# Optimization experiments

Hardware: AMD Instinct MI355X
Metric: run time of the kernel (lower is better)

Reference implementation:

```python
import jax, jax.numpy as jnp
import numpy as np

B, F, E, V = 8192, 16, 32, 100000
D, H1, H2 = 8, 1024, 512
IN = F * E  # 512
EPS = 1e-5


def _bn(x, gamma, beta):
    # x: [D, B, H]; training-mode BatchNorm1d per domain over batch axis (biased var)
    mean = jnp.mean(x, axis=1, keepdims=True)
    var = jnp.mean((x - mean) ** 2, axis=1, keepdims=True)
    return (x - mean) * jax.lax.rsqrt(var + EPS) * gamma[:, None, :] + beta[:, None, :]


def setup_inputs() -> dict:
    key = jax.random.key(0)
    ks = jax.random.split(key, 12)
    feat_ids = jax.random.randint(ks[0], (B, F), 0, V)
    domain_id = jax.random.randint(ks[1], (B,), 0, D)
    emb_tables = jax.random.normal(ks[2], (F, V, E), jnp.float32) * 0.02
    s1 = 1.0 / np.sqrt(IN)
    s2 = 1.0 / np.sqrt(H1)
    s3 = 1.0 / np.sqrt(H2)
    return {
        "feat_ids": feat_ids,
        "domain_id": domain_id,
        "emb_tables": emb_tables,
        "W1": jax.random.uniform(ks[3], (D, H1, IN), jnp.float32, -s1, s1),
        "b1": jax.random.uniform(ks[4], (D, H1), jnp.float32, -s1, s1),
        "g1": jnp.ones((D, H1), jnp.float32),
        "be1": jnp.zeros((D, H1), jnp.float32),
        "W2": jax.random.uniform(ks[5], (D, H2, H1), jnp.float32, -s2, s2),
        "b2": jax.random.uniform(ks[6], (D, H2), jnp.float32, -s2, s2),
        "g2": jnp.ones((D, H2), jnp.float32),
        "be2": jnp.zeros((D, H2), jnp.float32),
        "W3": jax.random.uniform(ks[7], (D, H2), jnp.float32, -s3, s3),
        "b3": jax.random.uniform(ks[8], (D,), jnp.float32, -s3, s3),
    }


def reference(feat_ids, domain_id, emb_tables, W1, b1, g1, be1, W2, b2, g2, be2, W3, b3):
    # embedding lookup per feature then concat -> [B, F*E]
    emb = jax.vmap(lambda tab, ids: tab[ids], in_axes=(0, 1), out_axes=1)(emb_tables, feat_ids)
    emb = emb.reshape(B, IN)
    # all-domain redundant MLP (as in original torch code)
    h = jnp.einsum('bf,dhf->dbh', emb, W1) + b1[:, None, :]          # [D,B,H1]
    h = jax.nn.relu(_bn(h, g1, be1))
    h = jnp.einsum('dbh,dkh->dbk', h, W2) + b2[:, None, :]           # [D,B,H2]
    h = jax.nn.relu(_bn(h, g2, be2))
    out = jax.nn.sigmoid(jnp.einsum('dbk,dk->db', h, W3) + b3[:, None])  # [D,B]
    # mask-select the row matching each sample's domain
    final = jnp.take_along_axis(out.T, domain_id[:, None], axis=1)[:, 0]  # [B]
    return final
```

## Files before the change

kernel.cpp:

```cpp
#include <hip/hip_runtime.h>
#include <hip/hip_bf16.h>

#define B_SZ   8192
#define F_CNT  16
#define E_DIM  32
#define V_CNT  100000
#define D_CNT  8
#define H1     1024
#define H2     512
#define IN_DIM 512
#define EPS_BN 1e-5f
#define SNIFF_THRESH 32

typedef __attribute__((ext_vector_type(8))) unsigned short ushort8;
typedef __attribute__((ext_vector_type(8))) short          frag_ab;
typedef __attribute__((ext_vector_type(4))) float          frag_cd;
typedef __attribute__((ext_vector_type(4))) float          float4v;

__device__ inline unsigned short f2b(float f) {
    unsigned int u = __builtin_bit_cast(unsigned int, f);
    unsigned int r = u + 0x7FFFu + ((u >> 16) & 1u);
    return (unsigned short)(r >> 16);
}
__device__ inline float b2f(unsigned short b) {
    return __builtin_bit_cast(float, (unsigned int)b << 16);
}

__global__ void k_sniff(const unsigned short* __restrict__ w, int nwords,
                        int* __restrict__ cnt) {
    int t = threadIdx.x;
    int c = 0;
    for (int i = t; i < nwords; i += 256) {
        unsigned int e = (w[i] >> 7) & 0xFFu;
        if (e >= 0x88u) c++;
    }
    __shared__ int red[256];
    red[t] = c; __syncthreads();
    for (int s = 128; s > 0; s >>= 1) { if (t < s) red[t] += red[t + s]; __syncthreads(); }
    if (t == 0) atomicAdd(cnt, red[0]);
}

__global__ void k_convert(const void* __restrict__ src, unsigned short* __restrict__ dst,
                          long n, const int* __restrict__ cnt) {
    long i = (long)blockIdx.x * 256 + threadIdx.x;
    if (i >= n) return;
    if (*cnt > SNIFF_THRESH) dst[i] = f2b(((const float*)src)[i]);
    else                     dst[i] = ((const unsigned short*)src)[i];
}

__global__ void k_gather(const int* __restrict__ feat_ids,
                         const void* __restrict__ tables,
                         unsigned short* __restrict__ emb,
                         const int* __restrict__ cnt) {
    int tid = blockIdx.x * 256 + threadIdx.x;
    int b = tid >> 6;
    int c = tid & 63;
    int f = c >> 2;
    int id = feat_ids[b * F_CNT + f];
    long base = ((long)f * V_CNT + id) * E_DIM + (c & 3) * 8;
    ushort8 o;
    if (*cnt > SNIFF_THRESH) {
        const float* s = (const float*)tables + base;
        float4v v0 = *(const float4v*)s;
        float4v v1 = *(const float4v*)(s + 4);
#pragma unroll
        for (int i = 0; i < 4; i++) { o[i] = f2b(v0[i]); o[i + 4] = f2b(v1[i]); }
    } else {
        o = *(const ushort8*)((const unsigned short*)tables + base);
    }
    *(ushort8*)(emb + (long)b * IN_DIM + c * 8) = o;
}

__global__ __launch_bounds__(256, 2)
void k_gemm(const unsigned short* __restrict__ A,
            const unsigned short* __restrict__ W,
            unsigned short* __restrict__ C,
            int M, int N, int K, long aBatchStride, int d0) {
    const int z  = blockIdx.z;
    const int m0 = blockIdx.x * 128;
    const int n0 = blockIdx.y * 128;
    const unsigned short* Ad = A + (long)z * aBatchStride;
    const unsigned short* Wd = W + (long)(d0 + z) * N * K;

    __shared__ unsigned short As[128][40];
    __shared__ unsigned short Bs[128][40];

    const int t    = threadIdx.x;
    const int wave = t >> 6;
    const int lane = t & 63;
    const int wm   = (wave & 1) << 6;
    const int wn   = (wave >> 1) << 6;
    const int q    = lane >> 4;
    const int lr   = lane & 15;

    const int r0   = t >> 2;
    const int koff = (t & 3) * 8;

    const unsigned short* aP0 = Ad + (long)(m0 + r0)      * K + koff;
    const unsigned short* aP1 = Ad + (long)(m0 + r0 + 64) * K + koff;
    const unsigned short* wP0 = Wd + (long)(n0 + r0)      * K + koff;
    const unsigned short* wP1 = Wd + (long)(n0 + r0 + 64) * K + koff;

    frag_cd acc[4][4];
#pragma unroll
    for (int i = 0; i < 4; i++)
#pragma unroll
        for (int j = 0; j < 4; j++)
            acc[i][j] = (frag_cd){0.f, 0.f, 0.f, 0.f};

    for (int k0 = 0; k0 < K; k0 += 32) {
        ushort8 a0 = *(const ushort8*)aP0;
        ushort8 a1 = *(const ushort8*)aP1;
        ushort8 b0 = *(const ushort8*)wP0;
        ushort8 b1 = *(const ushort8*)wP1;
        aP0 += 32; aP1 += 32; wP0 += 32; wP1 += 32;
        *(ushort8*)&As[r0][koff]      = a0;
        *(ushort8*)&As[r0 + 64][koff] = a1;
        *(ushort8*)&Bs[r0][koff]      = b0;
        *(ushort8*)&Bs[r0 + 64][koff] = b1;
        __syncthreads();

        frag_ab af[4], bf[4];
#pragma unroll
        for (int i = 0; i < 4; i++) {
            af[i] = *(const frag_ab*)&As[wm + i * 16 + lr][q * 8];
            bf[i] = *(const frag_ab*)&Bs[wn + i * 16 + lr][q * 8];
        }
#pragma unroll
        for (int i = 0; i < 4; i++)
#pragma unroll
            for (int j = 0; j < 4; j++)
                acc[i][j] = __builtin_amdgcn_mfma_f32_16x16x32_bf16(af[i], bf[j], acc[i][j], 0, 0, 0);
        __syncthreads();
    }

    unsigned short* Cd = C + (long)z * M * N;
#pragma unroll
    for (int i = 0; i < 4; i++) {
        int row = m0 + wm + i * 16 + q * 4;
#pragma unroll
        for (int j = 0; j < 4; j++) {
            int col = n0 + wn + j * 16 + lr;
#pragma unroll
            for (int r = 0; r < 4; r++)
                Cd[(long)(row + r) * N + col] = f2b(acc[i][j][r]);
        }
    }
}

__global__ void k_stats(const unsigned short* __restrict__ P, int H,
                        float* __restrict__ gsum, float* __restrict__ gsq, int d0) {
    const int z   = blockIdx.z;
    const int j0  = blockIdx.x * 128;
    const int seg = blockIdx.y;
    const int t = threadIdx.x;
    const int c = t & 15, r = t >> 4;
    const unsigned short* base = P + ((long)z * B_SZ + seg * 1024) * H + j0 + c * 8;
    float s[8], q[8];
#pragma unroll
    for (int i = 0; i < 8; i++) { s[i] = 0.f; q[i] = 0.f; }
    for (int b = r; b < 1024; b += 16) {
        ushort8 v = *(const ushort8*)(base + (long)b * H);
#pragma unroll
        for (int i = 0; i < 8; i++) { float x = b2f(v[i]); s[i] += x; q[i] += x * x; }
    }
    __shared__ float red[16][128];
#pragma unroll
    for (int i = 0; i < 8; i++) red[r][c * 8 + i] = s[i];
    __syncthreads();
    if (t < 128) {
        float a = 0.f;
#pragma unroll
        for (int rr = 0; rr < 16; rr++) a += red[rr][t];
        atomicAdd(&gsum[(d0 + z) * H + j0 + t], a);
    }
    __syncthreads();
#pragma unroll
    for (int i = 0; i < 8; i++) red[r][c * 8 + i] = q[i];
    __syncthreads();
    if (t < 128) {
        float a = 0.f;
#pragma unroll
        for (int rr = 0; rr < 16; rr++) a += red[rr][t];
        atomicAdd(&gsq[(d0 + z) * H + j0 + t], a);
    }
}

__global__ void k_finalize(const float* __restrict__ gsum, const float* __restrict__ gsq,
                           const void* __restrict__ g, const void* __restrict__ be,
                           float* __restrict__ scale, float* __restrict__ shift, int n,
                           int gOff, const int* __restrict__ cnt) {
    int i = blockIdx.x * 256 + threadIdx.x;
    if (i >= n) return;
    float gv, bv;
    if (*cnt > SNIFF_THRESH) {
        gv = ((const float*)g)[gOff + i];
        bv = ((const float*)be)[gOff + i];
    } else {
        gv = b2f(((const unsigned short*)g)[gOff + i]);
        bv = b2f(((const unsigned short*)be)[gOff + i]);
    }
    float mean = gsum[i] * (1.0f / B_SZ);
    float var  = gsq[i] * (1.0f / B_SZ) - mean * mean;
    float sc   = gv * rsqrtf(var + EPS_BN);
    scale[i] = sc;
    shift[i] = bv - mean * sc;
}

__global__ void k_bn_apply(const unsigned short* __restrict__ P,
                           const float* __restrict__ scale, const float* __restrict__ shift,
                           unsigned short* __restrict__ Out, int H, int d0) {
    long tid = (long)blockIdx.x * 256 + threadIdx.x;
    long off = tid * 8;
    int j  = (int)(off % H);
    int dj = ((int)(off / ((long)B_SZ * H)) + d0) * H + j;
    ushort8 v = *(const ushort8*)(P + off);
    float4v sc0 = *(const float4v*)(scale + dj);
    float4v sc1 = *(const float4v*)(scale + dj + 4);
    float4v sh0 = *(const float4v*)(shift + dj);
    float4v sh1 = *(const float4v*)(shift + dj + 4);
    ushort8 o;
#pragma unroll
    for (int i = 0; i < 8; i++) {
        float scv = (i < 4) ? sc0[i] : sc1[i - 4];
        float shv = (i < 4) ? sh0[i] : sh1[i - 4];
        float x = b2f(v[i]) * scv + shv;
        o[i] = f2b(fmaxf(x, 0.f));
    }
    *(ushort8*)(Out + off) = o;
}

__global__ void k_final(const unsigned short* __restrict__ h2c,
                        const int* __restrict__ domain_id,
                        const float* __restrict__ scale2, const float* __restrict__ shift2,
                        const unsigned short* __restrict__ W3, const unsigned short* __restrict__ b3,
                        void* __restrict__ out, int d0, int nc,
                        const int* __restrict__ cnt) {
    int wave = threadIdx.x >> 6, lane = threadIdx.x & 63;
    int b = blockIdx.x * 4 + wave;
    int d = domain_id[b];
    if (d < d0 || d >= d0 + nc) return;
    int o = d * H2 + lane * 8;
    ushort8 v = *(const ushort8*)(h2c + ((long)(d - d0) * B_SZ + b) * H2 + lane * 8);
    ushort8 w = *(const ushort8*)(W3 + o);
    float sum = 0.f;
#pragma unroll
    for (int i = 0; i < 8; i++) {
        float x = b2f(v[i]) * scale2[o + i] + shift2[o + i];
        sum += fmaxf(x, 0.f) * b2f(w[i]);
    }
#pragma unroll
    for (int off = 32; off > 0; off >>= 1) sum += __shfl_xor(sum, off, 64);
    if (lane == 0) {
        float res = 1.f / (1.f + expf(-(sum + b2f(b3[d]))));
        if (*cnt > SNIFF_THRESH) ((float*)out)[b] = res;
        else                     ((unsigned short*)out)[b] = f2b(res);
    }
}

__global__ void k_zero(float* __restrict__ p, int n) {
    int i = blockIdx.x * 256 + threadIdx.x;
    if (i < n) p[i] = 0.f;
}

__global__ void k_sentinel(float* __restrict__ out, int n) {
    int i = blockIdx.x * 256 + threadIdx.x;
    if (i < n) out[i] = 0.25f;
}

extern "C" void kernel_launch(void* const* d_in, const int* in_sizes, int n_in,
                              void* d_out, int out_size, void* d_ws, size_t ws_size,
                              hipStream_t stream) {
    const int* feat_ids  = (const int*)d_in[0];
    const int* domain_id = (const int*)d_in[1];
    const void* tables = d_in[2];
    const void* W1  = d_in[3];
    const void* g1  = d_in[5];
    const void* be1 = d_in[6];
    const void* W2  = d_in[7];
    const void* g2  = d_in[9];
    const void* be2 = d_in[10];
    const void* W3  = d_in[11];
    const void* b3  = d_in[12];

    char* ws = (char*)d_ws;
    float* gsum1  = (float*)ws;
    float* gsq1   = gsum1 + 8192;
    float* gsum2  = gsq1 + 8192;
    float* gsq2   = gsum2 + 4096;
    float* scale1 = gsq2 + 4096;
    float* shift1 = scale1 + 8192;
    float* scale2 = shift1 + 8192;
    float* shift2 = scale2 + 4096;
    int*   cntF   = (int*)(shift2 + 4096);
    unsigned short* W1c = (unsigned short*)(ws + (1L  << 20));
    unsigned short* W2c = (unsigned short*)(ws + (9L  << 20));
    unsigned short* W3c = (unsigned short*)(ws + (17L << 20));
    unsigned short* b3c = W3c + D_CNT * H2;
    unsigned short* emb = (unsigned short*)(ws + (18L << 20));

    const long h1Elems = (long)B_SZ * H1;
    const long h2Elems = (long)B_SZ * H2;
    const long perDom  = (h1Elems + h2Elems) * 2;
    const long baseOff = 26L << 20;
    int NC = 0;
    for (int cand = 8; cand >= 1; cand >>= 1)
        if (baseOff + (long)cand * perDom <= (long)ws_size) { NC = cand; break; }
    if (NC == 0) {
        k_sentinel<<<dim3((out_size + 255) / 256), dim3(256), 0, stream>>>(
            (float*)d_out, out_size);
        return;
    }
    unsigned short* h1c = (unsigned short*)(ws + baseOff);
    unsigned short* h2c = h1c + (long)NC * h1Elems;

    k_zero<<<dim3(193), dim3(256), 0, stream>>>(gsum1, 49184);
    k_sniff<<<dim3(1), dim3(256), 0, stream>>>((const unsigned short*)W1, 4096, cntF);
    k_convert<<<dim3(16384), dim3(256), 0, stream>>>(W1, W1c, (long)D_CNT * H1 * IN_DIM, cntF);
    k_convert<<<dim3(16384), dim3(256), 0, stream>>>(W2, W2c, (long)D_CNT * H2 * H1, cntF);
    k_convert<<<dim3(16),    dim3(256), 0, stream>>>(W3, W3c, (long)D_CNT * H2, cntF);
    k_convert<<<dim3(1),     dim3(256), 0, stream>>>(b3, b3c, (long)D_CNT, cntF);
    k_gather<<<dim3(2048), dim3(256), 0, stream>>>(feat_ids, tables, emb, cntF);

    for (int d0 = 0; d0 < D_CNT; d0 += NC) {
        k_gemm<<<dim3(64, 8, NC), dim3(256), 0, stream>>>(
            emb, W1c, h1c, 8192, 1024, 512, 0L, d0);
        k_stats<<<dim3(8, 8, NC), dim3(256), 0, stream>>>(h1c, H1, gsum1, gsq1, d0);
        k_finalize<<<dim3(NC * 4), dim3(256), 0, stream>>>(
            gsum1 + d0 * H1, gsq1 + d0 * H1, g1, be1,
            scale1 + d0 * H1, shift1 + d0 * H1, NC * H1, d0 * H1, cntF);
        k_bn_apply<<<dim3(NC * 4096), dim3(256), 0, stream>>>(
            h1c, scale1, shift1, h1c, H1, d0);
        k_gemm<<<dim3(64, 4, NC), dim3(256), 0, stream>>>(
            h1c, W2c, h2c, 8192, 512, 1024, h1Elems, d0);
        k_stats<<<dim3(4, 8, NC), dim3(256), 0, stream>>>(h2c, H2, gsum2, gsq2, d0);
        k_finalize<<<dim3(NC * 2), dim3(256), 0, stream>>>(
            gsum2 + d0 * H2, gsq2 + d0 * H2, g2, be2,
            scale2 + d0 * H2, shift2 + d0 * H2, NC * H2, d0 * H2, cntF);
        k_final<<<dim3(2048), dim3(256), 0, stream>>>(
            h2c, domain_id, scale2, shift2, W3c, b3c, d_out, d0, NC, cntF);
    }
}
```

Before: 555.5 us.

## Fuse BN statistics into GEMM epilogue, use direct-to-LDS loads, drop dtype sniffing

Result: faster. 500.2 us (-9.9%).

```diff
diff --git a/kernel.cpp b/kernel.cpp
--- a/kernel.cpp
+++ b/kernel.cpp
@@ -10,7 +10,6 @@
 #define H2     512
 #define IN_DIM 512
 #define EPS_BN 1e-5f
-#define SNIFF_THRESH 32
 
 typedef __attribute__((ext_vector_type(8))) unsigned short ushort8;
 typedef __attribute__((ext_vector_type(8))) short          frag_ab;
@@ -26,48 +25,37 @@
     return __builtin_bit_cast(float, (unsigned int)b << 16);
 }
 
-__global__ void k_sniff(const unsigned short* __restrict__ w, int nwords,
-                        int* __restrict__ cnt) {
-    int t = threadIdx.x;
-    int c = 0;
-    for (int i = t; i < nwords; i += 256) {
-        unsigned int e = (w[i] >> 7) & 0xFFu;
-        if (e >= 0x88u) c++;
-    }
-    __shared__ int red[256];
-    red[t] = c; __syncthreads();
-    for (int s = 128; s > 0; s >>= 1) { if (t < s) red[t] += red[t + s]; __syncthreads(); }
-    if (t == 0) atomicAdd(cnt, red[0]);
-}
-
-__global__ void k_convert(const void* __restrict__ src, unsigned short* __restrict__ dst,
-                          long n, const int* __restrict__ cnt) {
-    long i = (long)blockIdx.x * 256 + threadIdx.x;
+__device__ inline void ld_lds16(const unsigned short* g, unsigned short* l) {
+    __builtin_amdgcn_global_load_lds(
+        (const __attribute__((address_space(1))) unsigned int*)g,
+        (__attribute__((address_space(3))) unsigned int*)l, 16, 0, 0);
+}
+
+__global__ void k_convert(const float* __restrict__ src, unsigned short* __restrict__ dst,
+                          long n) {
+    long i = ((long)blockIdx.x * 256 + threadIdx.x) * 4;
     if (i >= n) return;
-    if (*cnt > SNIFF_THRESH) dst[i] = f2b(((const float*)src)[i]);
-    else                     dst[i] = ((const unsigned short*)src)[i];
+    float4v v = *(const float4v*)(src + i);
+    dst[i]     = f2b(v[0]);
+    dst[i + 1] = f2b(v[1]);
+    dst[i + 2] = f2b(v[2]);
+    dst[i + 3] = f2b(v[3]);
 }
 
 __global__ void k_gather(const int* __restrict__ feat_ids,
-                         const void* __restrict__ tables,
-                         unsigned short* __restrict__ emb,
-                         const int* __restrict__ cnt) {
+                         const float* __restrict__ tables,
+                         unsigned short* __restrict__ emb) {
     int tid = blockIdx.x * 256 + threadIdx.x;
     int b = tid >> 6;
     int c = tid & 63;
     int f = c >> 2;
     int id = feat_ids[b * F_CNT + f];
-    long base = ((long)f * V_CNT + id) * E_DIM + (c & 3) * 8;
+    const float* s = tables + ((long)f * V_CNT + id) * E_DIM + (c & 3) * 8;
+    float4v v0 = *(const float4v*)s;
+    float4v v1 = *(const float4v*)(s + 4);
     ushort8 o;
-    if (*cnt > SNIFF_THRESH) {
-        const float* s = (const float*)tables + base;
-        float4v v0 = *(const float4v*)s;
-        float4v v1 = *(const float4v*)(s + 4);
-#pragma unroll
-        for (int i = 0; i < 4; i++) { o[i] = f2b(v0[i]); o[i + 4] = f2b(v1[i]); }
-    } else {
-        o = *(const ushort8*)((const unsigned short*)tables + base);
-    }
+#pragma unroll
+    for (int i = 0; i < 4; i++) { o[i] = f2b(v0[i]); o[i + 4] = f2b(v1[i]); }
     *(ushort8*)(emb + (long)b * IN_DIM + c * 8) = o;
 }
 
@@ -75,6 +63,7 @@
 void k_gemm(const unsigned short* __restrict__ A,
             const unsigned short* __restrict__ W,
             unsigned short* __restrict__ C,
+            float* __restrict__ gsum, float* __restrict__ gsq,
             int M, int N, int K, long aBatchStride, int d0) {
     const int z  = blockIdx.z;
     const int m0 = blockIdx.x * 128;
@@ -82,8 +71,8 @@
     const unsigned short* Ad = A + (long)z * aBatchStride;
     const unsigned short* Wd = W + (long)(d0 + z) * N * K;
 
-    __shared__ unsigned short As[128][40];
-    __shared__ unsigned short Bs[128][40];
+    __shared__ unsigned short As[128 * 32];
+    __shared__ unsigned short Bs[128 * 32];
 
     const int t    = threadIdx.x;
     const int wave = t >> 6;
@@ -93,13 +82,16 @@
     const int q    = lane >> 4;
     const int lr   = lane & 15;
 
-    const int r0   = t >> 2;
-    const int koff = (t & 3) * 8;
-
-    const unsigned short* aP0 = Ad + (long)(m0 + r0)      * K + koff;
-    const unsigned short* aP1 = Ad + (long)(m0 + r0 + 64) * K + koff;
-    const unsigned short* wP0 = Wd + (long)(n0 + r0)      * K + koff;
-    const unsigned short* wP1 = Wd + (long)(n0 + r0 + 64) * K + koff;
+    const int srow = lane >> 2;
+    const int scol = (lane & 3) * 8;
+    const unsigned short* aG0 = Ad + (long)(m0 + wave * 32 + srow) * K + scol;
+    const unsigned short* aG1 = aG0 + 16 * (long)K;
+    const unsigned short* wG0 = Wd + (long)(n0 + wave * 32 + srow) * K + scol;
+    const unsigned short* wG1 = wG0 + 16 * (long)K;
+    unsigned short* aL0 = &As[(wave * 32) * 32];
+    unsigned short* aL1 = &As[(wave * 32 + 16) * 32];
+    unsigned short* wL0 = &Bs[(wave * 32) * 32];
+    unsigned short* wL1 = &Bs[(wave * 32 + 16) * 32];
 
     frag_cd acc[4][4];
 #pragma unroll
@@ -109,22 +101,17 @@
             acc[i][j] = (frag_cd){0.f, 0.f, 0.f, 0.f};
 
     for (int k0 = 0; k0 < K; k0 += 32) {
-        ushort8 a0 = *(const ushort8*)aP0;
-        ushort8 a1 = *(const ushort8*)aP1;
-        ushort8 b0 = *(const ushort8*)wP0;
-        ushort8 b1 = *(const ushort8*)wP1;
-        aP0 += 32; aP1 += 32; wP0 += 32; wP1 += 32;
-        *(ushort8*)&As[r0][koff]      = a0;
-        *(ushort8*)&As[r0 + 64][koff] = a1;
-        *(ushort8*)&Bs[r0][koff]      = b0;
-        *(ushort8*)&Bs[r0 + 64][koff] = b1;
+        ld_lds16(aG0 + k0, aL0);
+        ld_lds16(aG1 + k0, aL1);
+        ld_lds16(wG0 + k0, wL0);
+        ld_lds16(wG1 + k0, wL1);
         __syncthreads();
 
         frag_ab af[4], bf[4];
 #pragma unroll
         for (int i = 0; i < 4; i++) {
-            af[i] = *(const frag_ab*)&As[wm + i * 16 + lr][q * 8];
-            bf[i] = *(const frag_ab*)&Bs[wn + i * 16 + lr][q * 8];
+            af[i] = *(const frag_ab*)&As[(wm + i * 16 + lr) * 32 + q * 8];
+            bf[i] = *(const frag_ab*)&Bs[(wn + i * 16 + lr) * 32 + q * 8];
         }
 #pragma unroll
         for (int i = 0; i < 4; i++)
@@ -135,6 +122,9 @@
     }
 
     unsigned short* Cd = C + (long)z * M * N;
+    float s[4], q2[4];
+#pragma unroll
+    for (int j = 0; j < 4; j++) { s[j] = 0.f; q2[j] = 0.f; }
 #pragma unroll
     for (int i = 0; i < 4; i++) {
         int row = m0 + wm + i * 16 + q * 4;
@@ -142,69 +132,40 @@
         for (int j = 0; j < 4; j++) {
             int col = n0 + wn + j * 16 + lr;
 #pragma unroll
-            for (int r = 0; r < 4; r++)
-                Cd[(long)(row + r) * N + col] = f2b(acc[i][j][r]);
+            for (int r = 0; r < 4; r++) {
+                float v = acc[i][j][r];
+                Cd[(long)(row + r) * N + col] = f2b(v);
+                s[j] += v; q2[j] += v * v;
+            }
         }
     }
-}
-
-__global__ void k_stats(const unsigned short* __restrict__ P, int H,
-                        float* __restrict__ gsum, float* __restrict__ gsq, int d0) {
-    const int z   = blockIdx.z;
-    const int j0  = blockIdx.x * 128;
-    const int seg = blockIdx.y;
-    const int t = threadIdx.x;
-    const int c = t & 15, r = t >> 4;
-    const unsigned short* base = P + ((long)z * B_SZ + seg * 1024) * H + j0 + c * 8;
-    float s[8], q[8];
-#pragma unroll
-    for (int i = 0; i < 8; i++) { s[i] = 0.f; q[i] = 0.f; }
-    for (int b = r; b < 1024; b += 16) {
-        ushort8 v = *(const ushort8*)(base + (long)b * H);
-#pragma unroll
-        for (int i = 0; i < 8; i++) { float x = b2f(v[i]); s[i] += x; q[i] += x * x; }
-    }
-    __shared__ float red[16][128];
-#pragma unroll
-    for (int i = 0; i < 8; i++) red[r][c * 8 + i] = s[i];
-    __syncthreads();
-    if (t < 128) {
-        float a = 0.f;
-#pragma unroll
-        for (int rr = 0; rr < 16; rr++) a += red[rr][t];
-        atomicAdd(&gsum[(d0 + z) * H + j0 + t], a);
-    }
-    __syncthreads();
-#pragma unroll
-    for (int i = 0; i < 8; i++) red[r][c * 8 + i] = q[i];
-    __syncthreads();
-    if (t < 128) {
-        float a = 0.f;
-#pragma unroll
-        for (int rr = 0; rr < 16; rr++) a += red[rr][t];
-        atomicAdd(&gsq[(d0 + z) * H + j0 + t], a);
+#pragma unroll
+    for (int j = 0; j < 4; j++) {
+        s[j]  += __shfl_xor(s[j], 16, 64);  s[j]  += __shfl_xor(s[j], 32, 64);
+        q2[j] += __shfl_xor(q2[j], 16, 64); q2[j] += __shfl_xor(q2[j], 32, 64);
+    }
+    if (lane < 16) {
+        float* gs = gsum + (long)(d0 + z) * N + n0 + wn;
+        float* gq = gsq  + (long)(d0 + z) * N + n0 + wn;
+#pragma unroll
+        for (int j = 0; j < 4; j++) {
+            atomicAdd(&gs[j * 16 + lane], s[j]);
+            atomicAdd(&gq[j * 16 + lane], q2[j]);
+        }
     }
 }
 
 __global__ void k_finalize(const float* __restrict__ gsum, const float* __restrict__ gsq,
-                           const void* __restrict__ g, const void* __restrict__ be,
+                           const float* __restrict__ g, const float* __restrict__ be,
                            float* __restrict__ scale, float* __restrict__ shift, int n,
-                           int gOff, const int* __restrict__ cnt) {
+                           int gOff) {
     int i = blockIdx.x * 256 + threadIdx.x;
     if (i >= n) return;
-    float gv, bv;
-    if (*cnt > SNIFF_THRESH) {
-        gv = ((const float*)g)[gOff + i];
-        bv = ((const float*)be)[gOff + i];
-    } else {
-        gv = b2f(((const unsigned short*)g)[gOff + i]);
-        bv = b2f(((const unsigned short*)be)[gOff + i]);
-    }
     float mean = gsum[i] * (1.0f / B_SZ);
     float var  = gsq[i] * (1.0f / B_SZ) - mean * mean;
-    float sc   = gv * rsqrtf(var + EPS_BN);
+    float sc   = g[gOff + i] * rsqrtf(var + EPS_BN);
     scale[i] = sc;
-    shift[i] = bv - mean * sc;
+    shift[i] = be[gOff + i] - mean * sc;
 }
 
 __global__ void k_bn_apply(const unsigned short* __restrict__ P,
@@ -234,8 +195,7 @@
                         const int* __restrict__ domain_id,
                         const float* __restrict__ scale2, const float* __restrict__ shift2,
                         const unsigned short* __restrict__ W3, const unsigned short* __restrict__ b3,
-                        void* __restrict__ out, int d0, int nc,
-                        const int* __restrict__ cnt) {
+                        float* __restrict__ out, int d0, int nc) {
     int wave = threadIdx.x >> 6, lane = threadIdx.x & 63;
     int b = blockIdx.x * 4 + wave;
     int d = domain_id[b];
@@ -251,11 +211,8 @@
     }
 #pragma unroll
     for (int off = 32; off > 0; off >>= 1) sum += __shfl_xor(sum, off, 64);
-    if (lane == 0) {
-        float res = 1.f / (1.f + expf(-(sum + b2f(b3[d]))));
-        if (*cnt > SNIFF_THRESH) ((float*)out)[b] = res;
-        else                     ((unsigned short*)out)[b] = f2b(res);
-    }
+    if (lane == 0)
+        out[b] = 1.f / (1.f + expf(-(sum + b2f(b3[d]))));
 }
 
 __global__ void k_zero(float* __restrict__ p, int n) {
@@ -271,17 +228,17 @@
 extern "C" void kernel_launch(void* const* d_in, const int* in_sizes, int n_in,
                               void* d_out, int out_size, void* d_ws, size_t ws_size,
                               hipStream_t stream) {
-    const int* feat_ids  = (const int*)d_in[0];
-    const int* domain_id = (const int*)d_in[1];
-    const void* tables = d_in[2];
-    const void* W1  = d_in[3];
-    const void* g1  = d_in[5];
-    const void* be1 = d_in[6];
-    const void* W2  = d_in[7];
-    const void* g2  = d_in[9];
-    const void* be2 = d_in[10];
-    const void* W3  = d_in[11];
-    const void* b3  = d_in[12];
+    const int*   feat_ids  = (const int*)d_in[0];
+    const int*   domain_id = (const int*)d_in[1];
+    const float* tables = (const float*)d_in[2];
+    const float* W1  = (const float*)d_in[3];
+    const float* g1  = (const float*)d_in[5];
+    const float* be1 = (const float*)d_in[6];
+    const float* W2  = (const float*)d_in[7];
+    const float* g2  = (const float*)d_in[9];
+    const float* be2 = (const float*)d_in[10];
+    const float* W3  = (const float*)d_in[11];
+    const float* b3  = (const float*)d_in[12];
 
     char* ws = (char*)d_ws;
     float* gsum1  = (float*)ws;
@@ -292,7 +249,6 @@
     float* shift1 = scale1 + 8192;
     float* scale2 = shift1 + 8192;
     float* shift2 = scale2 + 4096;
-    int*   cntF   = (int*)(shift2 + 4096);
     unsigned short* W1c = (unsigned short*)(ws + (1L  << 20));
     unsigned short* W2c = (unsigned short*)(ws + (9L  << 20));
     unsigned short* W3c = (unsigned short*)(ws + (17L << 20));
@@ -314,30 +270,27 @@
     unsigned short* h1c = (unsigned short*)(ws + baseOff);
     unsigned short* h2c = h1c + (long)NC * h1Elems;
 
-    k_zero<<<dim3(193), dim3(256), 0, stream>>>(gsum1, 49184);
-    k_sniff<<<dim3(1), dim3(256), 0, stream>>>((const unsigned short*)W1, 4096, cntF);
-    k_convert<<<dim3(16384), dim3(256), 0, stream>>>(W1, W1c, (long)D_CNT * H1 * IN_DIM, cntF);
-    k_convert<<<dim3(16384), dim3(256), 0, stream>>>(W2, W2c, (long)D_CNT * H2 * H1, cntF);
-    k_convert<<<dim3(16),    dim3(256), 0, stream>>>(W3, W3c, (long)D_CNT * H2, cntF);
-    k_convert<<<dim3(1),     dim3(256), 0, stream>>>(b3, b3c, (long)D_CNT, cntF);
-    k_gather<<<dim3(2048), dim3(256), 0, stream>>>(feat_ids, tables, emb, cntF);
+    k_zero<<<dim3(96), dim3(256), 0, stream>>>(gsum1, 24576);
+    k_convert<<<dim3(4096), dim3(256), 0, stream>>>(W1, W1c, (long)D_CNT * H1 * IN_DIM);
+    k_convert<<<dim3(4096), dim3(256), 0, stream>>>(W2, W2c, (long)D_CNT * H2 * H1);
+    k_convert<<<dim3(4),    dim3(256), 0, stream>>>(W3, W3c, (long)D_CNT * H2);
+    k_convert<<<dim3(1),    dim3(2),   0, stream>>>(b3, b3c, (long)D_CNT);
+    k_gather<<<dim3(2048), dim3(256), 0, stream>>>(feat_ids, tables, emb);
 
     for (int d0 = 0; d0 < D_CNT; d0 += NC) {
         k_gemm<<<dim3(64, 8, NC), dim3(256), 0, stream>>>(
-            emb, W1c, h1c, 8192, 1024, 512, 0L, d0);
-        k_stats<<<dim3(8, 8, NC), dim3(256), 0, stream>>>(h1c, H1, gsum1, gsq1, d0);
+            emb, W1c, h1c, gsum1, gsq1, 8192, 1024, 512, 0L, d0);
         k_finalize<<<dim3(NC * 4), dim3(256), 0, stream>>>(
             gsum1 + d0 * H1, gsq1 + d0 * H1, g1, be1,
-            scale1 + d0 * H1, shift1 + d0 * H1, NC * H1, d0 * H1, cntF);
+            scale1 + d0 * H1, shift1 + d0 * H1, NC * H1, d0 * H1);
         k_bn_apply<<<dim3(NC * 4096), dim3(256), 0, stream>>>(
             h1c, scale1, shift1, h1c, H1, d0);
         k_gemm<<<dim3(64, 4, NC), dim3(256), 0, stream>>>(
-            h1c, W2c, h2c, 8192, 512, 1024, h1Elems, d0);
-        k_stats<<<dim3(4, 8, NC), dim3(256), 0, stream>>>(h2c, H2, gsum2, gsq2, d0);
+            h1c, W2c, h2c, gsum2, gsq2, 8192, 512, 1024, h1Elems, d0);
         k_finalize<<<dim3(NC * 2), dim3(256), 0, stream>>>(
             gsum2 + d0 * H2, gsq2 + d0 * H2, g2, be2,
-            scale2 + d0 * H2, shift2 + d0 * H2, NC * H2, d0 * H2, cntF);
+            scale2 + d0 * H2, shift2 + d0 * H2, NC * H2, d0 * H2);
         k_final<<<dim3(2048), dim3(256), 0, stream>>>(
-            h2c, domain_id, scale2, shift2, W3c, b3c, d_out, d0, NC, cntF);
-    }
-}
+            h2c, domain_id, scale2, shift2, W3c, b3c, (float*)d_out, d0, NC);
+    }
+}
```
